# Performance work log

Hardware: AMD Instinct MI355X
Metric: run time of the kernel (lower is better)

Reference implementation:

```python
import jax, jax.numpy as jnp
import numpy as np

B, S, D, H, E, TOP_K = 4, 2048, 1024, 2048, 8, 2


def setup_inputs() -> dict:
    key = jax.random.key(0)
    ks = jax.random.split(key, 5)
    scale_d = 1.0 / np.sqrt(D)
    scale_h = 1.0 / np.sqrt(H)
    return {
        "x": jax.random.normal(ks[0], (B, S, D), dtype=jnp.float32),
        "gate_w": jax.random.normal(ks[1], (D, E), dtype=jnp.float32) * scale_d,
        "w1": jax.random.normal(ks[2], (E, D, H), dtype=jnp.float32) * scale_d,
        "w2": jax.random.normal(ks[3], (E, D, H), dtype=jnp.float32) * scale_d,
        "w3": jax.random.normal(ks[4], (E, H, D), dtype=jnp.float32) * scale_h,
    }


def reference(x, gate_w, w1, w2, w3):
    # Gating: softmax over experts, keep top-k probs, renormalize.
    gate_scores = jax.nn.softmax(x @ gate_w, axis=-1)          # [B,S,E]
    top_vals, top_idx = jax.lax.top_k(gate_scores, TOP_K)      # [B,S,K]
    mask = (jax.nn.one_hot(top_idx, E, dtype=x.dtype) * top_vals[..., None]).sum(axis=-2)  # [B,S,E]
    weights = mask / (mask.sum(axis=-1, keepdims=True) + 1e-9)
    # Dense SwiGLU over ALL experts (faithful to the original ModuleList loop).
    g = jax.nn.silu(jnp.einsum('bsd,edh->bseh', x, w1)) * jnp.einsum('bsd,edh->bseh', x, w2)  # [B,S,E,H]
    expert_out = jnp.einsum('bseh,ehd->bsed', g, w3)           # [B,S,E,D]
    # Masked weighted combine (dropout is identity in eval / p=0).
    return jnp.einsum('bse,bsed->bsd', weights, expert_out)    # [B,S,D]
```

## Files before the change

kernel.cpp:

```cpp
#include <hip/hip_runtime.h>

#define T_TOK 8192
#define DDIM 1024
#define HDIM 2048
#define NEXP 8

typedef __attribute__((ext_vector_type(8))) short short8;
typedef __attribute__((ext_vector_type(4))) float f32x4;

#define WAITV8 asm volatile("s_waitcnt vmcnt(8)" ::: "memory")
#define WAITV0 asm volatile("s_waitcnt vmcnt(0)" ::: "memory")
#define WAITL0 asm volatile("s_waitcnt lgkmcnt(0)" ::: "memory")
#define SCHEDB __builtin_amdgcn_sched_barrier(0)
#define BARRIER __builtin_amdgcn_s_barrier()

__device__ __forceinline__ unsigned short f2bf(float f) {
  unsigned int u = __builtin_bit_cast(unsigned int, f);
  u += 0x7fffu + ((u >> 16) & 1u);
  return (unsigned short)(u >> 16);
}
__device__ __forceinline__ float bf2f(unsigned short h) {
  unsigned int u = ((unsigned int)h) << 16;
  return __builtin_bit_cast(float, u);
}
__device__ __forceinline__ void gload16(const void* g, void* l) {
  __builtin_amdgcn_global_load_lds((const __attribute__((address_space(1))) void*)g,
                                   (__attribute__((address_space(3))) void*)l, 16, 0, 0);
}
__device__ __forceinline__ int imin(int a, int b) { return a < b ? a : b; }

__global__ __launch_bounds__(256) void cvt_kernel(const float* __restrict__ in,
                                                  unsigned short* __restrict__ out, int n) {
  int i = (blockIdx.x * 256 + threadIdx.x) * 8;
  int stride = gridDim.x * 256 * 8;
  for (; i < n; i += stride) {
    float4 a = *(const float4*)(in + i);
    float4 b = *(const float4*)(in + i + 4);
    alignas(16) unsigned short t[8] = {f2bf(a.x), f2bf(a.y), f2bf(a.z), f2bf(a.w),
                                       f2bf(b.x), f2bf(b.y), f2bf(b.z), f2bf(b.w)};
    *(uint4*)(out + i) = *(const uint4*)t;
  }
}

__global__ __launch_bounds__(256) void tcvt_kernel(const float* __restrict__ in,
                                                   unsigned short* __restrict__ out,
                                                   int R, int C, size_t outEstride,
                                                   int perm, int s16) {
  int e = blockIdx.z;
  int rb = blockIdx.y * 64, cb = blockIdx.x * 64;
  const float* inE = in + (size_t)e * R * C;
  unsigned short* outE = out + (size_t)e * outEstride;
  __shared__ float tile[64][65];
  int tid = threadIdx.x;
  #pragma unroll
  for (int i = 0; i < 4; ++i) {
    int f = tid + i * 256;
    int r = f >> 4, c4 = (f & 15) << 2;
    float4 v = *(const float4*)(inE + (size_t)(rb + r) * C + cb + c4);
    tile[r][c4] = v.x; tile[r][c4 + 1] = v.y; tile[r][c4 + 2] = v.z; tile[r][c4 + 3] = v.w;
  }
  __syncthreads();
  #pragma unroll
  for (int i = 0; i < 2; ++i) {
    int g = tid + i * 256;
    int oc = g >> 3;
    int r8 = (g & 7) << 3;
    alignas(16) unsigned short tmp[8];
    #pragma unroll
    for (int j = 0; j < 8; ++j) tmp[j] = f2bf(tile[r8 + j][oc]);
    int orow = cb + oc;
    int orow2 = perm ? (32 * (orow >> 4) + (orow & 15) + s16) : orow;
    *(uint4*)(outE + (size_t)orow2 * R + rb + r8) = *(const uint4*)tmp;
  }
}

__global__ __launch_bounds__(256) void gate_kernel(const float* __restrict__ x,
                                                   const float* __restrict__ gw,
                                                   int* __restrict__ t_exp,
                                                   float* __restrict__ t_w) {
  int t = blockIdx.x * 4 + (threadIdx.x >> 6);
  int lane = threadIdx.x & 63;
  const float* xp = x + (size_t)t * DDIM;
  float acc[NEXP];
  #pragma unroll
  for (int e = 0; e < NEXP; ++e) acc[e] = 0.f;
  for (int i = 0; i < DDIM / 64; ++i) {
    int d = i * 64 + lane;
    float xv = xp[d];
    const float* g = gw + d * NEXP;
    #pragma unroll
    for (int e = 0; e < NEXP; ++e) acc[e] += xv * g[e];
  }
  #pragma unroll
  for (int off = 32; off > 0; off >>= 1) {
    #pragma unroll
    for (int e = 0; e < NEXP; ++e) acc[e] += __shfl_xor(acc[e], off, 64);
  }
  float mx = acc[0];
  #pragma unroll
  for (int e = 1; e < NEXP; ++e) mx = fmaxf(mx, acc[e]);
  float p[NEXP]; float S = 0.f;
  #pragma unroll
  for (int e = 0; e < NEXP; ++e) { p[e] = expf(acc[e] - mx); S += p[e]; }
  int i0 = 0; float v0 = p[0];
  #pragma unroll
  for (int e = 1; e < NEXP; ++e) if (p[e] > v0) { v0 = p[e]; i0 = e; }
  int i1 = -1; float v1 = -1.f;
  #pragma unroll
  for (int e = 0; e < NEXP; ++e) if (e != i0 && p[e] > v1) { v1 = p[e]; i1 = e; }
  float pv0 = v0 / S, pv1 = v1 / S;
  float denom = pv0 + pv1 + 1e-9f;
  if (lane == 0) {
    t_exp[t * 2] = i0; t_exp[t * 2 + 1] = i1;
    t_w[t * 2] = pv0 / denom; t_w[t * 2 + 1] = pv1 / denom;
  }
}

__global__ __launch_bounds__(1024) void partition_kernel(
    const int* __restrict__ t_exp, const float* __restrict__ t_w,
    int* __restrict__ ctrl, int* __restrict__ row_tok,
    float* __restrict__ row_w, int* __restrict__ inv_row) {
  int tid = threadIdx.x;
  int wv = tid >> 6, lane = tid & 63;
  __shared__ int wtot[16][8];
  __shared__ int wbase[16][8];
  __shared__ int soff[8];

  int t0 = tid * 8;
  int exps[16];
  int c[8];
  #pragma unroll
  for (int e = 0; e < 8; ++e) c[e] = 0;
  #pragma unroll
  for (int s = 0; s < 16; ++s) {
    exps[s] = t_exp[t0 * 2 + s];
    #pragma unroll
    for (int e = 0; e < 8; ++e) c[e] += (exps[s] == e);
  }
  int inc[8];
  #pragma unroll
  for (int e = 0; e < 8; ++e) inc[e] = c[e];
  #pragma unroll
  for (int d = 1; d < 64; d <<= 1) {
    #pragma unroll
    for (int e = 0; e < 8; ++e) {
      int v = __shfl_up(inc[e], d, 64);
      if (lane >= d) inc[e] += v;
    }
  }
  if (lane == 63) {
    #pragma unroll
    for (int e = 0; e < 8; ++e) wtot[wv][e] = inc[e];
  }
  __syncthreads();
  if (wv == 0 && lane < 16) {
    #pragma unroll
    for (int e = 0; e < 8; ++e) {
      int b = 0;
      for (int w = 0; w < 16; ++w)
        if (w < lane) b += wtot[w][e];
      wbase[lane][e] = b;
    }
  }
  __syncthreads();
  if (tid == 0) {
    int o = 0;
    #pragma unroll
    for (int e = 0; e < 8; ++e) {
      int tot = wbase[15][e] + wtot[15][e];
      ctrl[e] = tot; ctrl[8 + e] = o; soff[e] = o; o += tot;
    }
  }
  __syncthreads();
  int base[8];
  #pragma unroll
  for (int e = 0; e < 8; ++e) base[e] = soff[e] + wbase[wv][e] + (inc[e] - c[e]);
  #pragma unroll
  for (int s = 0; s < 16; ++s) {
    int ee = exps[s];
    float w = t_w[t0 * 2 + s];
    int pos = 0;
    #pragma unroll
    for (int e = 0; e < 8; ++e)
      if (ee == e) { pos = base[e]; base[e] = base[e] + 1; }
    row_tok[pos] = t0 + (s >> 1);
    row_w[pos] = w;
    inv_row[t0 * 2 + s] = pos;
  }
}


#define KSTEP(T_, NT_) do {                                                \
    int buf_ = (T_) & 3;                                                   \
    WAITV8;                                                                \
    BARRIER;                                                               \
    int tc_ = imin((T_) + 3, (NT_) - 1);                                   \
    STG(tc_ & 3, tc_);                                                     \
    short8 av[8], bv[4];                                                   \
    _Pragma("unroll")                                                      \
    for (int n = 0; n < 4; ++n)                                            \
      bv[n] = *(const short8*)(&lds[buf_][1][0] + bOff + n * 512);         \
    _Pragma("unroll")                                                      \
    for (int m = 0; m < 8; ++m)                                            \
      av[m] = *(const short8*)(&lds[buf_][0][0] + aOff + m * 512);         \
    __builtin_amdgcn_s_setprio(1);                                         \
    _Pragma("unroll")                                                      \
    for (int m = 0; m < 8; ++m)                                            \
      _Pragma("unroll")                                                    \
      for (int n = 0; n < 4; ++n)                                          \
        acc[m][n] = __builtin_amdgcn_mfma_f32_16x16x32_bf16(av[m], bv[n], acc[m][n], 0, 0, 0); \
    __builtin_amdgcn_s_setprio(0);                                         \
    WAITL0;                                                                \
} while (0)

#define K_PIPELINE(NT_)                                                    \
  WAITV0;                                                                  \
  STG(0, 0); STG(1, 1); STG(2, 2);                                         \
  _Pragma("unroll 1")                                                      \
  for (int t = 0; t < (NT_); ++t) { KSTEP(t, (NT_)); }

__global__ __launch_bounds__(512, 1) void gemm1_kernel(
    const unsigned short* __restrict__ xbf,
    const unsigned short* __restrict__ w12t,
    const int* __restrict__ row_tok, const float* __restrict__ row_w,
    const int* __restrict__ ctrl, unsigned short* __restrict__ G) {
  int bid = blockIdx.x;
  int e = bid & 7;
  int j = bid >> 3;
  int nt = ((j >> 5) << 2) | (j & 3);
  int mt0 = (j >> 2) & 7;
  int cnt = ctrl[e];
  if (mt0 * 256 >= cnt) return;
  int off = ctrl[8 + e];

  __shared__ unsigned short lds[4][2][8192];

  int tid = threadIdx.x, lane = tid & 63;
  const unsigned short* w12e = w12t + (size_t)e * (4096 * 1024);

  int sr = tid >> 2;
  int cS8 = ((tid & 3) ^ ((sr >> 1) & 3)) * 8;
  const unsigned short* bQ0 = w12e + (size_t)(nt * 256 + sr) * 1024 + cS8;
  const unsigned short* bQ1 = w12e + (size_t)(nt * 256 + 128 + sr) * 1024 + cS8;

  int wid = tid >> 6, wr = wid >> 2, wc = wid & 3;
  int lr16 = lane & 15, hi = lane >> 4;
  int koff = (hi ^ ((lr16 >> 1) & 3)) * 8;
  int aOff = (wr * 128 + lr16) * 32 + koff;
  int bOff = (wc * 64 + lr16) * 32 + koff;

#define STG(SB, T_) do {                                                   \
    gload16(aQ0 + (T_) * 32, &lds[SB][0][0] + tid * 8);                    \
    gload16(aQ1 + (T_) * 32, &lds[SB][0][0] + 4096 + tid * 8);             \
    gload16(bQ0 + (T_) * 32, &lds[SB][1][0] + tid * 8);                    \
    gload16(bQ1 + (T_) * 32, &lds[SB][1][0] + 4096 + tid * 8); } while (0)

  #pragma unroll 1
  for (int mt = mt0; mt * 256 < cnt; mt += 8) {
    int tokA = row_tok[off + imin(mt * 256 + sr, cnt - 1)];
    int tokB = row_tok[off + imin(mt * 256 + 128 + sr, cnt - 1)];
    const unsigned short* aQ0 = xbf + (size_t)tokA * 1024 + cS8;
    const unsigned short* aQ1 = xbf + (size_t)tokB * 1024 + cS8;

    f32x4 z = {0.f, 0.f, 0.f, 0.f};
    f32x4 acc[8][4];
    #pragma unroll
    for (int m = 0; m < 8; ++m)
      #pragma unroll
      for (int n = 0; n < 4; ++n) acc[m][n] = z;

    K_PIPELINE(32)

    #pragma unroll
    for (int m = 0; m < 8; ++m)
      #pragma unroll
      for (int jj = 0; jj < 4; ++jj) {
        int rl = mt * 256 + wr * 128 + m * 16 + hi * 4 + jj;
        if (rl < cnt) {
          float wrj = row_w[off + rl];
          size_t base = (size_t)(off + rl) * HDIM + nt * 128 + wc * 32 + lr16;
          float h1 = acc[m][0][jj], h2 = acc[m][1][jj];
          G[base] = f2bf((h1 / (1.f + __expf(-h1))) * h2 * wrj);
          h1 = acc[m][2][jj]; h2 = acc[m][3][jj];
          G[base + 16] = f2bf((h1 / (1.f + __expf(-h1))) * h2 * wrj);
        }
      }
  }
#undef STG
}

__global__ __launch_bounds__(512, 1) void gemm2_kernel(
    const unsigned short* __restrict__ G,
    const unsigned short* __restrict__ w3t,
    const int* __restrict__ ctrl, unsigned short* __restrict__ Y) {
  int bid = blockIdx.x;
  int e = bid & 7;
  int j = bid >> 3;
  int nt = j >> 3;
  int mt0 = j & 7;
  int cnt = ctrl[e];
  if (mt0 * 256 >= cnt) return;
  int off = ctrl[8 + e];

  __shared__ unsigned short lds[4][2][8192];

  int tid = threadIdx.x, lane = tid & 63;
  const unsigned short* w3e = w3t + (size_t)e * (1024 * 2048);

  int sr = tid >> 2;
  int cS8 = ((tid & 3) ^ ((sr >> 1) & 3)) * 8;
  const unsigned short* bQ0 = w3e + (size_t)(nt * 256 + sr) * 2048 + cS8;
  const unsigned short* bQ1 = w3e + (size_t)(nt * 256 + 128 + sr) * 2048 + cS8;

  int wid = tid >> 6, wr = wid >> 2, wc = wid & 3;
  int lr16 = lane & 15, hi = lane >> 4;
  int koff = (hi ^ ((lr16 >> 1) & 3)) * 8;
  int aOff = (wr * 128 + lr16) * 32 + koff;
  int bOff = (wc * 64 + lr16) * 32 + koff;

#define STG(SB, T_) do {                                                   \
    gload16(aQ0 + (T_) * 32, &lds[SB][0][0] + tid * 8);                    \
    gload16(aQ1 + (T_) * 32, &lds[SB][0][0] + 4096 + tid * 8);             \
    gload16(bQ0 + (T_) * 32, &lds[SB][1][0] + tid * 8);                    \
    gload16(bQ1 + (T_) * 32, &lds[SB][1][0] + 4096 + tid * 8); } while (0)

  #pragma unroll 1
  for (int mt = mt0; mt * 256 < cnt; mt += 8) {
    const unsigned short* aQ0 =
        G + (size_t)(off + imin(mt * 256 + sr, cnt - 1)) * 2048 + cS8;
    const unsigned short* aQ1 =
        G + (size_t)(off + imin(mt * 256 + 128 + sr, cnt - 1)) * 2048 + cS8;

    f32x4 z = {0.f, 0.f, 0.f, 0.f};
    f32x4 acc[8][4];
    #pragma unroll
    for (int m = 0; m < 8; ++m)
      #pragma unroll
      for (int n = 0; n < 4; ++n) acc[m][n] = z;

    K_PIPELINE(64)

    #pragma unroll
    for (int m = 0; m < 8; ++m)
      #pragma unroll
      for (int jj = 0; jj < 4; ++jj) {
        int rl = mt * 256 + wr * 128 + m * 16 + hi * 4 + jj;
        if (rl < cnt) {
          size_t yrow = (size_t)(off + rl) * DDIM + nt * 256 + wc * 64 + lr16;
          #pragma unroll
          for (int n = 0; n < 4; ++n) Y[yrow + n * 16] = f2bf(acc[m][n][jj]);
        }
      }
  }
#undef STG
}

__global__ __launch_bounds__(256) void combine_kernel(const unsigned short* __restrict__ Y,
                                                      const int* __restrict__ inv_row,
                                                      float* __restrict__ out) {
  int gid = blockIdx.x * 256 + threadIdx.x;
  int t = gid >> 7;
  int cidx = (gid & 127) * 8;
  int rA = inv_row[t * 2], rB = inv_row[t * 2 + 1];
  uint4 va = *(const uint4*)(Y + (size_t)rA * DDIM + cidx);
  uint4 vb = *(const uint4*)(Y + (size_t)rB * DDIM + cidx);
  const unsigned short* pa = (const unsigned short*)&va;
  const unsigned short* pb = (const unsigned short*)&vb;
  float4 o0, o1;
  o0.x = bf2f(pa[0]) + bf2f(pb[0]); o0.y = bf2f(pa[1]) + bf2f(pb[1]);
  o0.z = bf2f(pa[2]) + bf2f(pb[2]); o0.w = bf2f(pa[3]) + bf2f(pb[3]);
  o1.x = bf2f(pa[4]) + bf2f(pb[4]); o1.y = bf2f(pa[5]) + bf2f(pb[5]);
  o1.z = bf2f(pa[6]) + bf2f(pb[6]); o1.w = bf2f(pa[7]) + bf2f(pb[7]);
  float* op = out + (size_t)t * DDIM + cidx;
  *(float4*)op = o0;
  *(float4*)(op + 4) = o1;
}

extern "C" void kernel_launch(void* const* d_in, const int* in_sizes, int n_in,
                              void* d_out, int out_size, void* d_ws, size_t ws_size,
                              hipStream_t stream) {
  const float* x  = (const float*)d_in[0];
  const float* gw = (const float*)d_in[1];
  const float* w1 = (const float*)d_in[2];
  const float* w2 = (const float*)d_in[3];
  const float* w3 = (const float*)d_in[4];
  float* out = (float*)d_out;
  char* ws = (char*)d_ws;

  unsigned short* xbf  = (unsigned short*)(ws + 0);
  unsigned short* w12t = (unsigned short*)(ws + 16777216);
  unsigned short* w3t  = (unsigned short*)(ws + 83886080);
  unsigned short* G    = (unsigned short*)(ws + 117440512);
  unsigned short* Y    = (unsigned short*)(ws + 184549376);
  int*   row_tok = (int*)  (ws + 218103808);
  float* row_w   = (float*)(ws + 218169344);
  int*   inv_row = (int*)  (ws + 218234880);
  int*   t_exp   = (int*)  (ws + 218300416);
  float* t_w     = (float*)(ws + 218365952);
  int*   ctrl    = (int*)  (ws + 218431488);

  cvt_kernel<<<4096, 256, 0, stream>>>(x, xbf, T_TOK * DDIM);
  tcvt_kernel<<<dim3(32, 16, 8), 256, 0, stream>>>(w1, w12t, 1024, 2048,
                                                   (size_t)4096 * 1024, 1, 0);
  tcvt_kernel<<<dim3(32, 16, 8), 256, 0, stream>>>(w2, w12t, 1024, 2048,
                                                   (size_t)4096 * 1024, 1, 16);
  tcvt_kernel<<<dim3(16, 32, 8), 256, 0, stream>>>(w3, w3t, 2048, 1024,
                                                   (size_t)1024 * 2048, 0, 0);

  gate_kernel<<<2048, 256, 0, stream>>>(x, gw, t_exp, t_w);
  partition_kernel<<<1, 1024, 0, stream>>>(t_exp, t_w, ctrl, row_tok, row_w, inv_row);

  gemm1_kernel<<<1024, 512, 0, stream>>>(xbf, w12t, row_tok, row_w, ctrl, G);
  gemm2_kernel<<<256, 512, 0, stream>>>(G, w3t, ctrl, Y);
  combine_kernel<<<4096, 256, 0, stream>>>(Y, inv_row, out);
}
```

Baseline: 400.2 us.

## Fuse x bf16 conversion into gate kernel and split overflow rows into tail GEMMs

Result: slower. 488.0 us (+21.9%).

```diff
diff --git a/kernel.cpp b/kernel.cpp
--- a/kernel.cpp
+++ b/kernel.cpp
@@ -9,6 +9,7 @@
 typedef __attribute__((ext_vector_type(4))) float f32x4;
 
 #define WAITV8 asm volatile("s_waitcnt vmcnt(8)" ::: "memory")
+#define WAITV10 asm volatile("s_waitcnt vmcnt(10)" ::: "memory")
 #define WAITV0 asm volatile("s_waitcnt vmcnt(0)" ::: "memory")
 #define WAITL0 asm volatile("s_waitcnt lgkmcnt(0)" ::: "memory")
 #define SCHEDB __builtin_amdgcn_sched_barrier(0)
@@ -28,19 +29,6 @@
                                    (__attribute__((address_space(3))) void*)l, 16, 0, 0);
 }
 __device__ __forceinline__ int imin(int a, int b) { return a < b ? a : b; }
-
-__global__ __launch_bounds__(256) void cvt_kernel(const float* __restrict__ in,
-                                                  unsigned short* __restrict__ out, int n) {
-  int i = (blockIdx.x * 256 + threadIdx.x) * 8;
-  int stride = gridDim.x * 256 * 8;
-  for (; i < n; i += stride) {
-    float4 a = *(const float4*)(in + i);
-    float4 b = *(const float4*)(in + i + 4);
-    alignas(16) unsigned short t[8] = {f2bf(a.x), f2bf(a.y), f2bf(a.z), f2bf(a.w),
-                                       f2bf(b.x), f2bf(b.y), f2bf(b.z), f2bf(b.w)};
-    *(uint4*)(out + i) = *(const uint4*)t;
-  }
-}
 
 __global__ __launch_bounds__(256) void tcvt_kernel(const float* __restrict__ in,
                                                    unsigned short* __restrict__ out,
@@ -77,16 +65,19 @@
 __global__ __launch_bounds__(256) void gate_kernel(const float* __restrict__ x,
                                                    const float* __restrict__ gw,
                                                    int* __restrict__ t_exp,
-                                                   float* __restrict__ t_w) {
+                                                   float* __restrict__ t_w,
+                                                   unsigned short* __restrict__ xbf) {
   int t = blockIdx.x * 4 + (threadIdx.x >> 6);
   int lane = threadIdx.x & 63;
   const float* xp = x + (size_t)t * DDIM;
+  unsigned short* xo = xbf + (size_t)t * DDIM;
   float acc[NEXP];
   #pragma unroll
   for (int e = 0; e < NEXP; ++e) acc[e] = 0.f;
   for (int i = 0; i < DDIM / 64; ++i) {
     int d = i * 64 + lane;
     float xv = xp[d];
+    xo[d] = f2bf(xv);
     const float* g = gw + d * NEXP;
     #pragma unroll
     for (int e = 0; e < NEXP; ++e) acc[e] += xv * g[e];
@@ -228,9 +219,9 @@
   int e = bid & 7;
   int j = bid >> 3;
   int nt = ((j >> 5) << 2) | (j & 3);
-  int mt0 = (j >> 2) & 7;
+  int mt = (j >> 2) & 7;
   int cnt = ctrl[e];
-  if (mt0 * 256 >= cnt) return;
+  if (mt * 256 >= cnt) return;
   int off = ctrl[8 + e];
 
   __shared__ unsigned short lds[4][2][8192];
@@ -249,33 +240,125 @@
   int aOff = (wr * 128 + lr16) * 32 + koff;
   int bOff = (wc * 64 + lr16) * 32 + koff;
 
+  int tokA = row_tok[off + imin(mt * 256 + sr, cnt - 1)];
+  int tokB = row_tok[off + imin(mt * 256 + 128 + sr, cnt - 1)];
+  const unsigned short* aQ0 = xbf + (size_t)tokA * 1024 + cS8;
+  const unsigned short* aQ1 = xbf + (size_t)tokB * 1024 + cS8;
+
 #define STG(SB, T_) do {                                                   \
     gload16(aQ0 + (T_) * 32, &lds[SB][0][0] + tid * 8);                    \
     gload16(aQ1 + (T_) * 32, &lds[SB][0][0] + 4096 + tid * 8);             \
     gload16(bQ0 + (T_) * 32, &lds[SB][1][0] + tid * 8);                    \
     gload16(bQ1 + (T_) * 32, &lds[SB][1][0] + 4096 + tid * 8); } while (0)
 
+  f32x4 z = {0.f, 0.f, 0.f, 0.f};
+  f32x4 acc[8][4];
+  #pragma unroll
+  for (int m = 0; m < 8; ++m)
+    #pragma unroll
+    for (int n = 0; n < 4; ++n) acc[m][n] = z;
+
+  K_PIPELINE(32)
+
+  #pragma unroll
+  for (int m = 0; m < 8; ++m)
+    #pragma unroll
+    for (int jj = 0; jj < 4; ++jj) {
+      int rl = mt * 256 + wr * 128 + m * 16 + hi * 4 + jj;
+      if (rl < cnt) {
+        float wrj = row_w[off + rl];
+        size_t base = (size_t)(off + rl) * HDIM + nt * 128 + wc * 32 + lr16;
+        float h1 = acc[m][0][jj], h2 = acc[m][1][jj];
+        G[base] = f2bf((h1 / (1.f + __expf(-h1))) * h2 * wrj);
+        h1 = acc[m][2][jj]; h2 = acc[m][3][jj];
+        G[base + 16] = f2bf((h1 / (1.f + __expf(-h1))) * h2 * wrj);
+      }
+    }
+#undef STG
+}
+
+__global__ __launch_bounds__(256, 1) void gemm1_tail_kernel(
+    const unsigned short* __restrict__ xbf,
+    const unsigned short* __restrict__ w12t,
+    const int* __restrict__ row_tok, const float* __restrict__ row_w,
+    const int* __restrict__ ctrl, unsigned short* __restrict__ G) {
+  int bid = blockIdx.x;
+  int e = bid & 7;
+  int nt = bid >> 3;
+  int cnt = ctrl[e];
+  if (cnt <= 2048) return;
+  int off = ctrl[8 + e];
+
+  __shared__ unsigned short ldsA[4][2048];
+  __shared__ unsigned short ldsB[4][8192];
+
+  int tid = threadIdx.x, lane = tid & 63;
+  const unsigned short* w12e = w12t + (size_t)e * (4096 * 1024);
+
+  int sr = tid >> 2;
+  int cS8 = ((tid & 3) ^ ((sr >> 1) & 3)) * 8;
+  const unsigned short* bQ[4];
+  #pragma unroll
+  for (int q = 0; q < 4; ++q)
+    bQ[q] = w12e + (size_t)(nt * 256 + q * 64 + sr) * 1024 + cS8;
+
+  int wc = (tid >> 6) & 3;
+  int lr16 = lane & 15, hi = lane >> 4;
+  int koff = (hi ^ ((lr16 >> 1) & 3)) * 8;
+  int aOff = lr16 * 32 + koff;
+  int bOff = (wc * 64 + lr16) * 32 + koff;
+
   #pragma unroll 1
-  for (int mt = mt0; mt * 256 < cnt; mt += 8) {
-    int tokA = row_tok[off + imin(mt * 256 + sr, cnt - 1)];
-    int tokB = row_tok[off + imin(mt * 256 + 128 + sr, cnt - 1)];
-    const unsigned short* aQ0 = xbf + (size_t)tokA * 1024 + cS8;
-    const unsigned short* aQ1 = xbf + (size_t)tokB * 1024 + cS8;
+  for (int r0 = 2048; r0 < cnt; r0 += 64) {
+    int tokA = row_tok[off + imin(r0 + sr, cnt - 1)];
+    const unsigned short* aP = xbf + (size_t)tokA * 1024 + cS8;
+
+#define STGT(SB, T_) do {                                                  \
+    gload16(aP + (T_) * 32, &ldsA[SB][0] + tid * 8);                       \
+    gload16(bQ[0] + (T_) * 32, &ldsB[SB][0] + tid * 8);                    \
+    gload16(bQ[1] + (T_) * 32, &ldsB[SB][0] + 2048 + tid * 8);             \
+    gload16(bQ[2] + (T_) * 32, &ldsB[SB][0] + 4096 + tid * 8);             \
+    gload16(bQ[3] + (T_) * 32, &ldsB[SB][0] + 6144 + tid * 8); } while (0)
 
     f32x4 z = {0.f, 0.f, 0.f, 0.f};
-    f32x4 acc[8][4];
-    #pragma unroll
-    for (int m = 0; m < 8; ++m)
+    f32x4 acc[4][4];
+    #pragma unroll
+    for (int m = 0; m < 4; ++m)
       #pragma unroll
       for (int n = 0; n < 4; ++n) acc[m][n] = z;
 
-    K_PIPELINE(32)
-
-    #pragma unroll
-    for (int m = 0; m < 8; ++m)
+    WAITV0;
+    STGT(0, 0); STGT(1, 1); STGT(2, 2);
+    #pragma unroll 1
+    for (int t = 0; t < 32; ++t) {
+      int buf = t & 3;
+      WAITV10;
+      BARRIER;
+      int tc = imin(t + 3, 31);
+      STGT(tc & 3, tc);
+      short8 av[4], bv[4];
+      #pragma unroll
+      for (int n = 0; n < 4; ++n)
+        bv[n] = *(const short8*)(&ldsB[buf][0] + bOff + n * 512);
+      #pragma unroll
+      for (int m = 0; m < 4; ++m)
+        av[m] = *(const short8*)(&ldsA[buf][0] + aOff + m * 512);
+      __builtin_amdgcn_s_setprio(1);
+      #pragma unroll
+      for (int m = 0; m < 4; ++m)
+        #pragma unroll
+        for (int n = 0; n < 4; ++n)
+          acc[m][n] = __builtin_amdgcn_mfma_f32_16x16x32_bf16(av[m], bv[n], acc[m][n], 0, 0, 0);
+      __builtin_amdgcn_s_setprio(0);
+      WAITL0;
+    }
+#undef STGT
+
+    #pragma unroll
+    for (int m = 0; m < 4; ++m)
       #pragma unroll
       for (int jj = 0; jj < 4; ++jj) {
-        int rl = mt * 256 + wr * 128 + m * 16 + hi * 4 + jj;
+        int rl = r0 + m * 16 + hi * 4 + jj;
         if (rl < cnt) {
           float wrj = row_w[off + rl];
           size_t base = (size_t)(off + rl) * HDIM + nt * 128 + wc * 32 + lr16;
@@ -285,8 +368,8 @@
           G[base + 16] = f2bf((h1 / (1.f + __expf(-h1))) * h2 * wrj);
         }
       }
-  }
-#undef STG
+    BARRIER;
+  }
 }
 
 __global__ __launch_bounds__(512, 1) void gemm2_kernel(
@@ -297,9 +380,9 @@
   int e = bid & 7;
   int j = bid >> 3;
   int nt = j >> 3;
-  int mt0 = j & 7;
+  int mt = j & 7;
   int cnt = ctrl[e];
-  if (mt0 * 256 >= cnt) return;
+  if (mt * 256 >= cnt) return;
   int off = ctrl[8 + e];
 
   __shared__ unsigned short lds[4][2][8192];
@@ -311,6 +394,8 @@
   int cS8 = ((tid & 3) ^ ((sr >> 1) & 3)) * 8;
   const unsigned short* bQ0 = w3e + (size_t)(nt * 256 + sr) * 2048 + cS8;
   const unsigned short* bQ1 = w3e + (size_t)(nt * 256 + 128 + sr) * 2048 + cS8;
+  const unsigned short* aQ0 = G + (size_t)(off + imin(mt * 256 + sr, cnt - 1)) * 2048 + cS8;
+  const unsigned short* aQ1 = G + (size_t)(off + imin(mt * 256 + 128 + sr, cnt - 1)) * 2048 + cS8;
 
   int wid = tid >> 6, wr = wid >> 2, wc = wid & 3;
   int lr16 = lane & 15, hi = lane >> 4;
@@ -324,35 +409,118 @@
     gload16(bQ0 + (T_) * 32, &lds[SB][1][0] + tid * 8);                    \
     gload16(bQ1 + (T_) * 32, &lds[SB][1][0] + 4096 + tid * 8); } while (0)
 
+  f32x4 z = {0.f, 0.f, 0.f, 0.f};
+  f32x4 acc[8][4];
+  #pragma unroll
+  for (int m = 0; m < 8; ++m)
+    #pragma unroll
+    for (int n = 0; n < 4; ++n) acc[m][n] = z;
+
+  K_PIPELINE(64)
+
+  #pragma unroll
+  for (int m = 0; m < 8; ++m)
+    #pragma unroll
+    for (int jj = 0; jj < 4; ++jj) {
+      int rl = mt * 256 + wr * 128 + m * 16 + hi * 4 + jj;
+      if (rl < cnt) {
+        size_t yrow = (size_t)(off + rl) * DDIM + nt * 256 + wc * 64 + lr16;
+        #pragma unroll
+        for (int n = 0; n < 4; ++n) Y[yrow + n * 16] = f2bf(acc[m][n][jj]);
+      }
+    }
+#undef STG
+}
+
+__global__ __launch_bounds__(256, 1) void gemm2_tail_kernel(
+    const unsigned short* __restrict__ G,
+    const unsigned short* __restrict__ w3t,
+    const int* __restrict__ ctrl, unsigned short* __restrict__ Y) {
+  int bid = blockIdx.x;
+  int e = bid & 7;
+  int nt = bid >> 3;
+  int cnt = ctrl[e];
+  if (cnt <= 2048) return;
+  int off = ctrl[8 + e];
+
+  __shared__ unsigned short ldsA[4][2048];
+  __shared__ unsigned short ldsB[4][8192];
+
+  int tid = threadIdx.x, lane = tid & 63;
+  const unsigned short* w3e = w3t + (size_t)e * (1024 * 2048);
+
+  int sr = tid >> 2;
+  int cS8 = ((tid & 3) ^ ((sr >> 1) & 3)) * 8;
+  const unsigned short* bQ[4];
+  #pragma unroll
+  for (int q = 0; q < 4; ++q)
+    bQ[q] = w3e + (size_t)(nt * 256 + q * 64 + sr) * 2048 + cS8;
+
+  int wc = (tid >> 6) & 3;
+  int lr16 = lane & 15, hi = lane >> 4;
+  int koff = (hi ^ ((lr16 >> 1) & 3)) * 8;
+  int aOff = lr16 * 32 + koff;
+  int bOff = (wc * 64 + lr16) * 32 + koff;
+
   #pragma unroll 1
-  for (int mt = mt0; mt * 256 < cnt; mt += 8) {
-    const unsigned short* aQ0 =
-        G + (size_t)(off + imin(mt * 256 + sr, cnt - 1)) * 2048 + cS8;
-    const unsigned short* aQ1 =
-        G + (size_t)(off + imin(mt * 256 + 128 + sr, cnt - 1)) * 2048 + cS8;
+  for (int r0 = 2048; r0 < cnt; r0 += 64) {
+    const unsigned short* aP =
+        G + (size_t)(off + imin(r0 + sr, cnt - 1)) * 2048 + cS8;
+
+#define STGT(SB, T_) do {                                                  \
+    gload16(aP + (T_) * 32, &ldsA[SB][0] + tid * 8);                       \
+    gload16(bQ[0] + (T_) * 32, &ldsB[SB][0] + tid * 8);                    \
+    gload16(bQ[1] + (T_) * 32, &ldsB[SB][0] + 2048 + tid * 8);             \
+    gload16(bQ[2] + (T_) * 32, &ldsB[SB][0] + 4096 + tid * 8);             \
+    gload16(bQ[3] + (T_) * 32, &ldsB[SB][0] + 6144 + tid * 8); } while (0)
 
     f32x4 z = {0.f, 0.f, 0.f, 0.f};
-    f32x4 acc[8][4];
-    #pragma unroll
-    for (int m = 0; m < 8; ++m)
+    f32x4 acc[4][4];
+    #pragma unroll
+    for (int m = 0; m < 4; ++m)
       #pragma unroll
       for (int n = 0; n < 4; ++n) acc[m][n] = z;
 
-    K_PIPELINE(64)
-
-    #pragma unroll
-    for (int m = 0; m < 8; ++m)
+    WAITV0;
+    STGT(0, 0); STGT(1, 1); STGT(2, 2);
+    #pragma unroll 1
+    for (int t = 0; t < 64; ++t) {
+      int buf = t & 3;
+      WAITV10;
+      BARRIER;
+      int tc = imin(t + 3, 63);
+      STGT(tc & 3, tc);
+      short8 av[4], bv[4];
+      #pragma unroll
+      for (int n = 0; n < 4; ++n)
+        bv[n] = *(const short8*)(&ldsB[buf][0] + bOff + n * 512);
+      #pragma unroll
+      for (int m = 0; m < 4; ++m)
+        av[m] = *(const short8*)(&ldsA[buf][0] + aOff + m * 512);
+      __builtin_amdgcn_s_setprio(1);
+      #pragma unroll
+      for (int m = 0; m < 4; ++m)
+        #pragma unroll
+        for (int n = 0; n < 4; ++n)
+          acc[m][n] = __builtin_amdgcn_mfma_f32_16x16x32_bf16(av[m], bv[n], acc[m][n], 0, 0, 0);
+      __builtin_amdgcn_s_setprio(0);
+      WAITL0;
+    }
+#undef STGT
+
+    #pragma unroll
+    for (int m = 0; m < 4; ++m)
       #pragma unroll
       for (int jj = 0; jj < 4; ++jj) {
-        int rl = mt * 256 + wr * 128 + m * 16 + hi * 4 + jj;
+        int rl = r0 + m * 16 + hi * 4 + jj;
         if (rl < cnt) {
           size_t yrow = (size_t)(off + rl) * DDIM + nt * 256 + wc * 64 + lr16;
           #pragma unroll
           for (int n = 0; n < 4; ++n) Y[yrow + n * 16] = f2bf(acc[m][n][jj]);
         }
       }
-  }
-#undef STG
+    BARRIER;
+  }
 }
 
 __global__ __launch_bounds__(256) void combine_kernel(const unsigned short* __restrict__ Y,
@@ -399,7 +567,6 @@
   float* t_w     = (float*)(ws + 218365952);
   int*   ctrl    = (int*)  (ws + 218431488);
 
-  cvt_kernel<<<4096, 256, 0, stream>>>(x, xbf, T_TOK * DDIM);
   tcvt_kernel<<<dim3(32, 16, 8), 256, 0, stream>>>(w1, w12t, 1024, 2048,
                                                    (size_t)4096 * 1024, 1, 0);
   tcvt_kernel<<<dim3(32, 16, 8), 256, 0, stream>>>(w2, w12t, 1024, 2048,
@@ -407,10 +574,12 @@
   tcvt_kernel<<<dim3(16, 32, 8), 256, 0, stream>>>(w3, w3t, 2048, 1024,
                                                    (size_t)1024 * 2048, 0, 0);
 
-  gate_kernel<<<2048, 256, 0, stream>>>(x, gw, t_exp, t_w);
+  gate_kernel<<<2048, 256, 0, stream>>>(x, gw, t_exp, t_w, xbf);
   partition_kernel<<<1, 1024, 0, stream>>>(t_exp, t_w, ctrl, row_tok, row_w, inv_row);
 
   gemm1_kernel<<<1024, 512, 0, stream>>>(xbf, w12t, row_tok, row_w, ctrl, G);
+  gemm1_tail_kernel<<<128, 256, 0, stream>>>(xbf, w12t, row_tok, row_w, ctrl, G);
   gemm2_kernel<<<256, 512, 0, stream>>>(G, w3t, ctrl, Y);
+  gemm2_tail_kernel<<<32, 256, 0, stream>>>(G, w3t, ctrl, Y);
   combine_kernel<<<4096, 256, 0, stream>>>(Y, inv_row, out);
 }
```

## Schedule MoE GEMMs via compact tile map, fuse x bf16 cast into gate

Applied to the files above, without the earlier changes.

Result: slower. 446.5 us (+11.6%).

```diff
diff --git a/kernel.cpp b/kernel.cpp
--- a/kernel.cpp
+++ b/kernel.cpp
@@ -9,9 +9,9 @@
 typedef __attribute__((ext_vector_type(4))) float f32x4;
 
 #define WAITV8 asm volatile("s_waitcnt vmcnt(8)" ::: "memory")
+#define WAITV6 asm volatile("s_waitcnt vmcnt(6)" ::: "memory")
 #define WAITV0 asm volatile("s_waitcnt vmcnt(0)" ::: "memory")
 #define WAITL0 asm volatile("s_waitcnt lgkmcnt(0)" ::: "memory")
-#define SCHEDB __builtin_amdgcn_sched_barrier(0)
 #define BARRIER __builtin_amdgcn_s_barrier()
 
 __device__ __forceinline__ unsigned short f2bf(float f) {
@@ -28,19 +28,6 @@
                                    (__attribute__((address_space(3))) void*)l, 16, 0, 0);
 }
 __device__ __forceinline__ int imin(int a, int b) { return a < b ? a : b; }
-
-__global__ __launch_bounds__(256) void cvt_kernel(const float* __restrict__ in,
-                                                  unsigned short* __restrict__ out, int n) {
-  int i = (blockIdx.x * 256 + threadIdx.x) * 8;
-  int stride = gridDim.x * 256 * 8;
-  for (; i < n; i += stride) {
-    float4 a = *(const float4*)(in + i);
-    float4 b = *(const float4*)(in + i + 4);
-    alignas(16) unsigned short t[8] = {f2bf(a.x), f2bf(a.y), f2bf(a.z), f2bf(a.w),
-                                       f2bf(b.x), f2bf(b.y), f2bf(b.z), f2bf(b.w)};
-    *(uint4*)(out + i) = *(const uint4*)t;
-  }
-}
 
 __global__ __launch_bounds__(256) void tcvt_kernel(const float* __restrict__ in,
                                                    unsigned short* __restrict__ out,
@@ -77,16 +64,19 @@
 __global__ __launch_bounds__(256) void gate_kernel(const float* __restrict__ x,
                                                    const float* __restrict__ gw,
                                                    int* __restrict__ t_exp,
-                                                   float* __restrict__ t_w) {
+                                                   float* __restrict__ t_w,
+                                                   unsigned short* __restrict__ xbf) {
   int t = blockIdx.x * 4 + (threadIdx.x >> 6);
   int lane = threadIdx.x & 63;
   const float* xp = x + (size_t)t * DDIM;
+  unsigned short* xo = xbf + (size_t)t * DDIM;
   float acc[NEXP];
   #pragma unroll
   for (int e = 0; e < NEXP; ++e) acc[e] = 0.f;
   for (int i = 0; i < DDIM / 64; ++i) {
     int d = i * 64 + lane;
     float xv = xp[d];
+    xo[d] = f2bf(xv);
     const float* g = gw + d * NEXP;
     #pragma unroll
     for (int e = 0; e < NEXP; ++e) acc[e] += xv * g[e];
@@ -119,7 +109,8 @@
 __global__ __launch_bounds__(1024) void partition_kernel(
     const int* __restrict__ t_exp, const float* __restrict__ t_w,
     int* __restrict__ ctrl, int* __restrict__ row_tok,
-    float* __restrict__ row_w, int* __restrict__ inv_row) {
+    float* __restrict__ row_w, int* __restrict__ inv_row,
+    int* __restrict__ tmap) {
   int tid = threadIdx.x;
   int wv = tid >> 6, lane = tid & 63;
   __shared__ int wtot[16][8];
@@ -186,6 +177,21 @@
     row_tok[pos] = t0 + (s >> 1);
     row_w[pos] = w;
     inv_row[t0 * 2 + s] = pos;
+  }
+  __syncthreads();
+  if (tid == 0) {
+    int T1 = 0, T2 = 0;
+    for (int e = 0; e < 8; ++e) {
+      int cnt = ctrl[e];
+      int n1 = (cnt + 255) >> 8;
+      for (int m = 0; m < n1; ++m) tmap[T1++] = (e << 8) | m;
+    }
+    for (int e = 0; e < 8; ++e) {
+      int cnt = ctrl[e];
+      int n2 = (cnt + 127) >> 7;
+      for (int m = 0; m < n2; ++m) tmap[128 + T2++] = (e << 8) | m;
+    }
+    ctrl[16] = T1; ctrl[17] = T2;
   }
 }
 
@@ -223,14 +229,15 @@
     const unsigned short* __restrict__ xbf,
     const unsigned short* __restrict__ w12t,
     const int* __restrict__ row_tok, const float* __restrict__ row_w,
-    const int* __restrict__ ctrl, unsigned short* __restrict__ G) {
+    const int* __restrict__ ctrl, const int* __restrict__ tmap,
+    unsigned short* __restrict__ G) {
   int bid = blockIdx.x;
-  int e = bid & 7;
-  int j = bid >> 3;
-  int nt = ((j >> 5) << 2) | (j & 3);
-  int mt0 = (j >> 2) & 7;
+  int nt = bid & 15;
+  int ti = bid >> 4;
+  if (ti >= ctrl[16]) return;
+  int pm = tmap[ti];
+  int e = pm >> 8, mt = pm & 255;
   int cnt = ctrl[e];
-  if (mt0 * 256 >= cnt) return;
   int off = ctrl[8 + e];
 
   __shared__ unsigned short lds[4][2][8192];
@@ -249,60 +256,59 @@
   int aOff = (wr * 128 + lr16) * 32 + koff;
   int bOff = (wc * 64 + lr16) * 32 + koff;
 
+  int tokA = row_tok[off + imin(mt * 256 + sr, cnt - 1)];
+  int tokB = row_tok[off + imin(mt * 256 + 128 + sr, cnt - 1)];
+  const unsigned short* aQ0 = xbf + (size_t)tokA * 1024 + cS8;
+  const unsigned short* aQ1 = xbf + (size_t)tokB * 1024 + cS8;
+
 #define STG(SB, T_) do {                                                   \
     gload16(aQ0 + (T_) * 32, &lds[SB][0][0] + tid * 8);                    \
     gload16(aQ1 + (T_) * 32, &lds[SB][0][0] + 4096 + tid * 8);             \
     gload16(bQ0 + (T_) * 32, &lds[SB][1][0] + tid * 8);                    \
     gload16(bQ1 + (T_) * 32, &lds[SB][1][0] + 4096 + tid * 8); } while (0)
 
-  #pragma unroll 1
-  for (int mt = mt0; mt * 256 < cnt; mt += 8) {
-    int tokA = row_tok[off + imin(mt * 256 + sr, cnt - 1)];
-    int tokB = row_tok[off + imin(mt * 256 + 128 + sr, cnt - 1)];
-    const unsigned short* aQ0 = xbf + (size_t)tokA * 1024 + cS8;
-    const unsigned short* aQ1 = xbf + (size_t)tokB * 1024 + cS8;
-
-    f32x4 z = {0.f, 0.f, 0.f, 0.f};
-    f32x4 acc[8][4];
-    #pragma unroll
-    for (int m = 0; m < 8; ++m)
-      #pragma unroll
-      for (int n = 0; n < 4; ++n) acc[m][n] = z;
-
-    K_PIPELINE(32)
-
-    #pragma unroll
-    for (int m = 0; m < 8; ++m)
-      #pragma unroll
-      for (int jj = 0; jj < 4; ++jj) {
-        int rl = mt * 256 + wr * 128 + m * 16 + hi * 4 + jj;
-        if (rl < cnt) {
-          float wrj = row_w[off + rl];
-          size_t base = (size_t)(off + rl) * HDIM + nt * 128 + wc * 32 + lr16;
-          float h1 = acc[m][0][jj], h2 = acc[m][1][jj];
-          G[base] = f2bf((h1 / (1.f + __expf(-h1))) * h2 * wrj);
-          h1 = acc[m][2][jj]; h2 = acc[m][3][jj];
-          G[base + 16] = f2bf((h1 / (1.f + __expf(-h1))) * h2 * wrj);
-        }
+  f32x4 z = {0.f, 0.f, 0.f, 0.f};
+  f32x4 acc[8][4];
+  #pragma unroll
+  for (int m = 0; m < 8; ++m)
+    #pragma unroll
+    for (int n = 0; n < 4; ++n) acc[m][n] = z;
+
+  K_PIPELINE(32)
+
+  #pragma unroll
+  for (int m = 0; m < 8; ++m)
+    #pragma unroll
+    for (int jj = 0; jj < 4; ++jj) {
+      int rl = mt * 256 + wr * 128 + m * 16 + hi * 4 + jj;
+      if (rl < cnt) {
+        float wrj = row_w[off + rl];
+        size_t base = (size_t)(off + rl) * HDIM + nt * 128 + wc * 32 + lr16;
+        float h1 = acc[m][0][jj], h2 = acc[m][1][jj];
+        G[base] = f2bf((h1 / (1.f + __expf(-h1))) * h2 * wrj);
+        h1 = acc[m][2][jj]; h2 = acc[m][3][jj];
+        G[base + 16] = f2bf((h1 / (1.f + __expf(-h1))) * h2 * wrj);
       }
-  }
+    }
 #undef STG
 }
 
 __global__ __launch_bounds__(512, 1) void gemm2_kernel(
     const unsigned short* __restrict__ G,
     const unsigned short* __restrict__ w3t,
-    const int* __restrict__ ctrl, unsigned short* __restrict__ Y) {
+    const int* __restrict__ ctrl, const int* __restrict__ tmap,
+    unsigned short* __restrict__ Y) {
   int bid = blockIdx.x;
-  int e = bid & 7;
-  int j = bid >> 3;
-  int nt = j >> 3;
-  int mt0 = j & 7;
+  int nt = bid & 3;
+  int ti = bid >> 2;
+  if (ti >= ctrl[17]) return;
+  int pm = tmap[ti];
+  int e = pm >> 8, mt = pm & 255;
   int cnt = ctrl[e];
-  if (mt0 * 256 >= cnt) return;
   int off = ctrl[8 + e];
 
-  __shared__ unsigned short lds[4][2][8192];
+  __shared__ unsigned short ldsA[4][4096];
+  __shared__ unsigned short ldsB[4][8192];
 
   int tid = threadIdx.x, lane = tid & 63;
   const unsigned short* w3e = w3t + (size_t)e * (1024 * 2048);
@@ -311,48 +317,65 @@
   int cS8 = ((tid & 3) ^ ((sr >> 1) & 3)) * 8;
   const unsigned short* bQ0 = w3e + (size_t)(nt * 256 + sr) * 2048 + cS8;
   const unsigned short* bQ1 = w3e + (size_t)(nt * 256 + 128 + sr) * 2048 + cS8;
+  const unsigned short* aQ0 =
+      G + (size_t)(off + imin(mt * 128 + sr, cnt - 1)) * 2048 + cS8;
 
   int wid = tid >> 6, wr = wid >> 2, wc = wid & 3;
   int lr16 = lane & 15, hi = lane >> 4;
   int koff = (hi ^ ((lr16 >> 1) & 3)) * 8;
-  int aOff = (wr * 128 + lr16) * 32 + koff;
+  int aOff = (wr * 64 + lr16) * 32 + koff;
   int bOff = (wc * 64 + lr16) * 32 + koff;
 
-#define STG(SB, T_) do {                                                   \
-    gload16(aQ0 + (T_) * 32, &lds[SB][0][0] + tid * 8);                    \
-    gload16(aQ1 + (T_) * 32, &lds[SB][0][0] + 4096 + tid * 8);             \
-    gload16(bQ0 + (T_) * 32, &lds[SB][1][0] + tid * 8);                    \
-    gload16(bQ1 + (T_) * 32, &lds[SB][1][0] + 4096 + tid * 8); } while (0)
-
+#define STG2(SB, T_) do {                                                  \
+    gload16(aQ0 + (T_) * 32, &ldsA[SB][0] + tid * 8);                      \
+    gload16(bQ0 + (T_) * 32, &ldsB[SB][0] + tid * 8);                      \
+    gload16(bQ1 + (T_) * 32, &ldsB[SB][0] + 4096 + tid * 8); } while (0)
+
+  f32x4 z = {0.f, 0.f, 0.f, 0.f};
+  f32x4 acc[4][4];
+  #pragma unroll
+  for (int m = 0; m < 4; ++m)
+    #pragma unroll
+    for (int n = 0; n < 4; ++n) acc[m][n] = z;
+
+  WAITV0;
+  STG2(0, 0); STG2(1, 1); STG2(2, 2);
   #pragma unroll 1
-  for (int mt = mt0; mt * 256 < cnt; mt += 8) {
-    const unsigned short* aQ0 =
-        G + (size_t)(off + imin(mt * 256 + sr, cnt - 1)) * 2048 + cS8;
-    const unsigned short* aQ1 =
-        G + (size_t)(off + imin(mt * 256 + 128 + sr, cnt - 1)) * 2048 + cS8;
-
-    f32x4 z = {0.f, 0.f, 0.f, 0.f};
-    f32x4 acc[8][4];
-    #pragma unroll
-    for (int m = 0; m < 8; ++m)
+  for (int t = 0; t < 64; ++t) {
+    int buf = t & 3;
+    WAITV6;
+    BARRIER;
+    int tc = imin(t + 3, 63);
+    STG2(tc & 3, tc);
+    short8 av[4], bv[4];
+    #pragma unroll
+    for (int n = 0; n < 4; ++n)
+      bv[n] = *(const short8*)(&ldsB[buf][0] + bOff + n * 512);
+    #pragma unroll
+    for (int m = 0; m < 4; ++m)
+      av[m] = *(const short8*)(&ldsA[buf][0] + aOff + m * 512);
+    __builtin_amdgcn_s_setprio(1);
+    #pragma unroll
+    for (int m = 0; m < 4; ++m)
       #pragma unroll
-      for (int n = 0; n < 4; ++n) acc[m][n] = z;
-
-    K_PIPELINE(64)
-
-    #pragma unroll
-    for (int m = 0; m < 8; ++m)
-      #pragma unroll
-      for (int jj = 0; jj < 4; ++jj) {
-        int rl = mt * 256 + wr * 128 + m * 16 + hi * 4 + jj;
-        if (rl < cnt) {
-          size_t yrow = (size_t)(off + rl) * DDIM + nt * 256 + wc * 64 + lr16;
-          #pragma unroll
-          for (int n = 0; n < 4; ++n) Y[yrow + n * 16] = f2bf(acc[m][n][jj]);
-        }
+      for (int n = 0; n < 4; ++n)
+        acc[m][n] = __builtin_amdgcn_mfma_f32_16x16x32_bf16(av[m], bv[n], acc[m][n], 0, 0, 0);
+    __builtin_amdgcn_s_setprio(0);
+    WAITL0;
+  }
+#undef STG2
+
+  #pragma unroll
+  for (int m = 0; m < 4; ++m)
+    #pragma unroll
+    for (int jj = 0; jj < 4; ++jj) {
+      int rl = mt * 128 + wr * 64 + m * 16 + hi * 4 + jj;
+      if (rl < cnt) {
+        size_t yrow = (size_t)(off + rl) * DDIM + nt * 256 + wc * 64 + lr16;
+        #pragma unroll
+        for (int n = 0; n < 4; ++n) Y[yrow + n * 16] = f2bf(acc[m][n][jj]);
       }
-  }
-#undef STG
+    }
 }
 
 __global__ __launch_bounds__(256) void combine_kernel(const unsigned short* __restrict__ Y,
@@ -399,7 +422,6 @@
   float* t_w     = (float*)(ws + 218365952);
   int*   ctrl    = (int*)  (ws + 218431488);
 
-  cvt_kernel<<<4096, 256, 0, stream>>>(x, xbf, T_TOK * DDIM);
   tcvt_kernel<<<dim3(32, 16, 8), 256, 0, stream>>>(w1, w12t, 1024, 2048,
                                                    (size_t)4096 * 1024, 1, 0);
   tcvt_kernel<<<dim3(32, 16, 8), 256, 0, stream>>>(w2, w12t, 1024, 2048,
@@ -407,10 +429,11 @@
   tcvt_kernel<<<dim3(16, 32, 8), 256, 0, stream>>>(w3, w3t, 2048, 1024,
                                                    (size_t)1024 * 2048, 0, 0);
 
-  gate_kernel<<<2048, 256, 0, stream>>>(x, gw, t_exp, t_w);
-  partition_kernel<<<1, 1024, 0, stream>>>(t_exp, t_w, ctrl, row_tok, row_w, inv_row);
-
-  gemm1_kernel<<<1024, 512, 0, stream>>>(xbf, w12t, row_tok, row_w, ctrl, G);
-  gemm2_kernel<<<256, 512, 0, stream>>>(G, w3t, ctrl, Y);
+  gate_kernel<<<2048, 256, 0, stream>>>(x, gw, t_exp, t_w, xbf);
+  partition_kernel<<<1, 1024, 0, stream>>>(t_exp, t_w, ctrl, row_tok, row_w,
+                                           inv_row, t_exp);
+
+  gemm1_kernel<<<1152, 512, 0, stream>>>(xbf, w12t, row_tok, row_w, ctrl, t_exp, G);
+  gemm2_kernel<<<544, 512, 0, stream>>>(G, w3t, ctrl, t_exp + 128, Y);
   combine_kernel<<<4096, 256, 0, stream>>>(Y, inv_row, out);
 }
```
